# Kernel tuning notes

Hardware: AMD Instinct MI355X
Metric: run time of the kernel (lower is better)

Reference implementation:

```python
import jax, jax.numpy as jnp
import numpy as np

N_NODES = 50000
N_EDGES = 600000
IN_DIM = 128
HID_DIM = 128


def setup_inputs() -> dict:
    key = jax.random.key(0)
    ks = jax.random.split(key, 6)
    x = jax.random.normal(ks[0], (N_NODES, IN_DIM), dtype=jnp.float32)
    edge_index = jax.random.randint(ks[1], (2, N_EDGES), 0, N_NODES, dtype=jnp.int32)
    # GCNConv linear weights (applied as x @ W) and biases
    W1 = jax.random.normal(ks[2], (IN_DIM, HID_DIM), dtype=jnp.float32) * (1.0 / np.sqrt(IN_DIM))
    b1 = jnp.zeros((HID_DIM,), dtype=jnp.float32)
    W2 = jax.random.normal(ks[3], (HID_DIM, HID_DIM), dtype=jnp.float32) * (1.0 / np.sqrt(HID_DIM))
    b2 = jnp.zeros((HID_DIM,), dtype=jnp.float32)
    return {"x": x, "edge_index": edge_index, "W1": W1, "b1": b1, "W2": W2, "b2": b2}


def _gcn_norm(edge_index, num_nodes):
    # add self-loops (edge_weight=None -> all ones), symmetric normalization
    loop = jnp.arange(num_nodes, dtype=edge_index.dtype)
    src = jnp.concatenate([edge_index[0], loop])  # [E+N]
    dst = jnp.concatenate([edge_index[1], loop])  # [E+N]
    ew = jnp.ones(src.shape[0], dtype=jnp.float32)
    deg = jax.ops.segment_sum(ew, dst, num_segments=num_nodes)  # in-degree incl. self-loop
    dinv = jnp.where(deg > 0, jax.lax.rsqrt(deg), 0.0)
    norm = dinv[src] * ew * dinv[dst]  # [E+N]
    return src, dst, norm


def _gcn_layer(z, W, b, src, dst, norm, num_nodes):
    h = z @ W  # [N, H] dense transform
    msg = h[src] * norm[:, None]  # gather + scale  [E+N, H]
    agg = jax.ops.segment_sum(msg, dst, num_segments=num_nodes)  # scatter-add [N, H]
    return agg + b


def reference(x, edge_index, W1, b1, W2, b2):
    num_nodes = x.shape[0]
    src, dst, norm = _gcn_norm(edge_index, num_nodes)
    z = jax.nn.relu(_gcn_layer(x, W1, b1, src, dst, norm, num_nodes))
    z = jax.nn.relu(_gcn_layer(z, W2, b2, src, dst, norm, num_nodes))
    return z
```

## Files before the change

### kernel.cpp

```cpp
#include <hip/hip_runtime.h>

#define NN 50000
#define NE 600000
#define DIM 128
#define CAP 40

#define OFF_CUR    0
#define OFF_DINV   200704
#define OFF_FLAG   401408
#define OFF_SRCL   401920
#define OFF_W1T    8401920
#define OFF_W2T    8434688
#define OFF_Y      8467456
#define OFF_Z1     21267968

typedef unsigned short u16;
typedef unsigned int u32;
typedef __attribute__((ext_vector_type(8))) short short8;
typedef __attribute__((ext_vector_type(4))) float floatx4;

__device__ __forceinline__ float bflo(u32 u) { return __uint_as_float(u << 16); }
__device__ __forceinline__ float bfhi(u32 u) { return __uint_as_float(u & 0xFFFF0000u); }
__device__ __forceinline__ u16 f2bf(float f) {
    u32 x = __float_as_uint(f);
    return (u16)((x + 0x7FFFu + ((x >> 16) & 1u)) >> 16);
}
__device__ __forceinline__ u32 pack2(float hi, float lo) {
    return ((u32)f2bf(hi) << 16) | (u32)f2bf(lo);
}

__global__ __launch_bounds__(256) void k_init(
    const int* __restrict__ ei, const float* __restrict__ W1,
    const float* __restrict__ W2, char* __restrict__ ws) {
    int* cur = (int*)(ws + OFF_CUR);
    int* flagw = (int*)(ws + OFF_FLAG);
    u16* W1t = (u16*)(ws + OFF_W1T);
    u16* W2t = (u16*)(ws + OFF_W2T);
    int b = blockIdx.x, tid = threadIdx.x;
    for (int i = b * 256 + tid; i < NN; i += 128 * 256) cur[i] = 0;
    const float* W = (b < 64) ? W1 : W2;
    u16* Wt = (b < 64) ? W1t : W2t;
    int e = (b & 63) * 256 + tid;
    int k = e >> 7, n = e & 127;
    Wt[n * DIM + k] = f2bf(W[e]);
    if (b == 0) {
        __shared__ int sc;
        if (tid == 0) sc = 0;
        __syncthreads();
        int lc = 0;
        for (int i = tid; i < 1024; i += 256) lc += (ei[2 * i + 1] != 0) ? 1 : 0;
        if (lc) atomicAdd(&sc, lc);
        __syncthreads();
        if (tid == 0) *flagw = (sc < 16) ? 1 : 0;
    }
}

__global__ __launch_bounds__(256) void k_fill(const int* __restrict__ ei,
                                              char* __restrict__ ws) {
    int* cur = (int*)(ws + OFF_CUR);
    int* srclist = (int*)(ws + OFF_SRCL);
    int is64 = *(const int*)(ws + OFF_FLAG);
    int i = blockIdx.x * 256 + threadIdx.x;
    if (i >= NE) return;
    int d = is64 ? ei[2 * (NE + i)] : ei[NE + i];
    if ((u32)d >= NN) return;
    int p = atomicAdd(&cur[d], 1);
    if (p < CAP) {
        int s = is64 ? ei[2 * i] : ei[i];
        srclist[d * CAP + p] = ((u32)s < NN) ? s : 0;
    }
}

__global__ __launch_bounds__(256) void k_scale(const float* __restrict__ x,
                                               char* __restrict__ ws) {
    const int* cur = (const int*)(ws + OFF_CUR);
    float* dinv = (float*)(ws + OFF_DINV);
    u32* y = (u32*)(ws + OFF_Y);
    int i = blockIdx.x * 256 + threadIdx.x;
    if (i >= NN * 32) return;
    int n = i >> 5;
    float dn = rsqrtf((float)(cur[n] + 1));
    if ((i & 31) == 0) dinv[n] = dn;
    float4 v = ((const float4*)x)[i];
    uint2 o;
    o.x = pack2(dn * v.y, dn * v.x);
    o.y = pack2(dn * v.w, dn * v.z);
    ((uint2*)y)[i] = o;
}

__global__ __launch_bounds__(256) void k_layer(
    const u32* __restrict__ y, const char* __restrict__ ws,
    const u16* __restrict__ Bt, const float* __restrict__ bias,
    void* __restrict__ out, int mode) {
    const int* cur = (const int*)(ws + OFF_CUR);
    const int* srclist = (const int*)(ws + OFF_SRCL);
    const float* dinv = (const float*)(ws + OFF_DINV);
    __shared__ u32 tl[16][68];
    int tid = threadIdx.x;
    int wv = tid >> 6, lane = tid & 63;
    int grp = lane >> 4, sl16 = lane & 15;
    int node0 = blockIdx.x << 4;
    int nn = wv * 4 + grp;
    int n = node0 + nn;
    int cnt = cur[n];
    cnt = cnt < CAP ? cnt : CAP;
    float dn = dinv[n];
    const int* sl = srclist + (size_t)n * CAP;
    int c1 = cnt > 0 ? cnt - 1 : 0;

    uint4 us = *(const uint4*)(y + (size_t)n * 64 + sl16 * 4);
    float a0 = bflo(us.x), a1 = bfhi(us.x), a2 = bflo(us.y), a3 = bfhi(us.y);
    float a4 = bflo(us.z), a5 = bfhi(us.z), a6 = bflo(us.w), a7 = bfhi(us.w);

    int mx = cnt;
    mx = max(mx, __shfl_xor(mx, 16));
    mx = max(mx, __shfl_xor(mx, 32));

#define SIDX(j) ((j) < cnt ? sl[(j) < c1 ? (j) : c1] : n)
#define ROW(s) (*(const uint4*)(y + (size_t)(s) * 64 + sl16 * 4))
#define MSK(j) (((j) < cnt) ? 0xFFFFFFFFu : 0u)
    if (mx > 0) {
        int s0 = SIDX(0), s1 = SIDX(1), s2 = SIDX(2), s3 = SIDX(3);
        u32 m0 = MSK(0), m1 = MSK(1), m2 = MSK(2), m3 = MSK(3);
        uint4 u0 = ROW(s0), u1 = ROW(s1), u2 = ROW(s2);
        int sF = s3;
#pragma unroll 2
        for (int i = 0; i < mx; ++i) {
            int sN = SIDX(i + 4);
            uint4 u3 = ROW(sF);
            u32 v;
            v = u0.x & m0; a0 += bflo(v); a1 += bfhi(v);
            v = u0.y & m0; a2 += bflo(v); a3 += bfhi(v);
            v = u0.z & m0; a4 += bflo(v); a5 += bfhi(v);
            v = u0.w & m0; a6 += bflo(v); a7 += bfhi(v);
            u0 = u1; u1 = u2; u2 = u3;
            m0 = m1; m1 = m2; m2 = m3; m3 = MSK(i + 4);
            sF = sN;
        }
    }
#undef SIDX
#undef ROW
#undef MSK
    uint4 o;
    o.x = pack2(dn * a1, dn * a0);
    o.y = pack2(dn * a3, dn * a2);
    o.z = pack2(dn * a5, dn * a4);
    o.w = pack2(dn * a7, dn * a6);
    *(uint4*)&tl[nn][sl16 * 4] = o;
    __syncthreads();

    int m = lane & 15, kg = lane >> 4;
    floatx4 acc[2];
    acc[0] = (floatx4){0.f, 0.f, 0.f, 0.f};
    acc[1] = (floatx4){0.f, 0.f, 0.f, 0.f};
#pragma unroll
    for (int kk = 0; kk < 4; ++kk) {
        int k0 = kk * 32 + kg * 8;
        short8 a = *(const short8*)&tl[m][kk * 16 + kg * 4];
#pragma unroll
        for (int j = 0; j < 2; ++j) {
            int nt = wv * 2 + j;
            short8 b = *(const short8*)(Bt + (size_t)(nt * 16 + m) * DIM + k0);
            acc[j] = __builtin_amdgcn_mfma_f32_16x16x32_bf16(a, b, acc[j], 0, 0, 0);
        }
    }
    float4 d4 = (mode == 0) ? *(const float4*)(dinv + node0 + kg * 4)
                            : make_float4(1.f, 1.f, 1.f, 1.f);
#pragma unroll
    for (int j = 0; j < 2; ++j) {
        int col = (wv * 2 + j) * 16 + m;
        float bv = bias[col];
#pragma unroll
        for (int r = 0; r < 4; ++r) {
            int row = node0 + kg * 4 + r;
            float v = acc[j][r] + bv;
            v = v > 0.f ? v : 0.f;
            if (mode == 0)
                ((u16*)out)[(size_t)row * DIM + col] = f2bf(v * (&d4.x)[r]);
            else
                ((float*)out)[(size_t)row * DIM + col] = v;
        }
    }
}

extern "C" void kernel_launch(void* const* d_in, const int* in_sizes, int n_in,
                              void* d_out, int out_size, void* d_ws, size_t ws_size,
                              hipStream_t stream) {
    (void)in_sizes; (void)n_in; (void)out_size; (void)ws_size;
    const float* x  = (const float*)d_in[0];
    const int*   ei = (const int*)d_in[1];
    const float* W1 = (const float*)d_in[2];
    const float* b1 = (const float*)d_in[3];
    const float* W2 = (const float*)d_in[4];
    const float* b2 = (const float*)d_in[5];
    char* ws = (char*)d_ws;

    u16* W1t = (u16*)(ws + OFF_W1T);
    u16* W2t = (u16*)(ws + OFF_W2T);
    u32* y   = (u32*)(ws + OFF_Y);
    u32* z1  = (u32*)(ws + OFF_Z1);

    k_init<<<128, 256, 0, stream>>>(ei, W1, W2, ws);
    k_fill<<<(NE + 255) / 256, 256, 0, stream>>>(ei, ws);
    k_scale<<<NN * 32 / 256, 256, 0, stream>>>(x, ws);
    k_layer<<<NN / 16, 256, 0, stream>>>(y, ws, W1t, b1, z1, 0);
    k_layer<<<NN / 16, 256, 0, stream>>>(z1, ws, W2t, b2, d_out, 1);
}
```

Measured before the change: 194.2 us.

## Fuse edge fill with bf16 packing and compute source degree scaling in layer one

Merges the CSR fill and x-to-bf16 pack kernels into one launch, which is possible because the pack no longer needs degrees: x is packed unscaled. The first layer instead reads each source node's count and applies rsqrt per gathered neighbor, and all dinv values are recomputed from counts, so the dinv array is gone. This saves a launch and a pass over the data, but adds a dependent gather of cur[src] plus an rsqrt per edge in layer one's inner loop.

```diff
diff --git a/kernel.cpp b/kernel.cpp
--- a/kernel.cpp
+++ b/kernel.cpp
@@ -6,7 +6,6 @@
 #define CAP 40
 
 #define OFF_CUR    0
-#define OFF_DINV   200704
 #define OFF_FLAG   401408
 #define OFF_SRCL   401920
 #define OFF_W1T    8401920
@@ -29,7 +28,7 @@
     return ((u32)f2bf(hi) << 16) | (u32)f2bf(lo);
 }
 
-__global__ __launch_bounds__(256) void k_init(
+__global__ __launch_bounds__(256) void k_z(
     const int* __restrict__ ei, const float* __restrict__ W1,
     const float* __restrict__ W2, char* __restrict__ ws) {
     int* cur = (int*)(ws + OFF_CUR);
@@ -55,37 +54,28 @@
     }
 }
 
-__global__ __launch_bounds__(256) void k_fill(const int* __restrict__ ei,
-                                              char* __restrict__ ws) {
+__global__ __launch_bounds__(256) void k_fillpack(const int* __restrict__ ei,
+                                                  const float* __restrict__ x,
+                                                  char* __restrict__ ws) {
     int* cur = (int*)(ws + OFF_CUR);
     int* srclist = (int*)(ws + OFF_SRCL);
-    int is64 = *(const int*)(ws + OFF_FLAG);
-    int i = blockIdx.x * 256 + threadIdx.x;
-    if (i >= NE) return;
-    int d = is64 ? ei[2 * (NE + i)] : ei[NE + i];
-    if ((u32)d >= NN) return;
-    int p = atomicAdd(&cur[d], 1);
-    if (p < CAP) {
-        int s = is64 ? ei[2 * i] : ei[i];
-        srclist[d * CAP + p] = ((u32)s < NN) ? s : 0;
-    }
-}
-
-__global__ __launch_bounds__(256) void k_scale(const float* __restrict__ x,
-                                               char* __restrict__ ws) {
-    const int* cur = (const int*)(ws + OFF_CUR);
-    float* dinv = (float*)(ws + OFF_DINV);
-    u32* y = (u32*)(ws + OFF_Y);
-    int i = blockIdx.x * 256 + threadIdx.x;
-    if (i >= NN * 32) return;
-    int n = i >> 5;
-    float dn = rsqrtf((float)(cur[n] + 1));
-    if ((i & 31) == 0) dinv[n] = dn;
-    float4 v = ((const float4*)x)[i];
+    int gid = blockIdx.x * 256 + threadIdx.x;
+    float4 v = ((const float4*)x)[gid];
     uint2 o;
-    o.x = pack2(dn * v.y, dn * v.x);
-    o.y = pack2(dn * v.w, dn * v.z);
-    ((uint2*)y)[i] = o;
+    o.x = pack2(v.y, v.x);
+    o.y = pack2(v.w, v.z);
+    ((uint2*)(ws + OFF_Y))[gid] = o;
+    if (gid < NE) {
+        int is64 = *(const int*)(ws + OFF_FLAG);
+        int d = is64 ? ei[2 * (NE + gid)] : ei[NE + gid];
+        if ((u32)d < NN) {
+            int p = atomicAdd(&cur[d], 1);
+            if (p < CAP) {
+                int s = is64 ? ei[2 * gid] : ei[gid];
+                srclist[d * CAP + p] = ((u32)s < NN) ? s : 0;
+            }
+        }
+    }
 }
 
 __global__ __launch_bounds__(256) void k_layer(
@@ -94,7 +84,6 @@
     void* __restrict__ out, int mode) {
     const int* cur = (const int*)(ws + OFF_CUR);
     const int* srclist = (const int*)(ws + OFF_SRCL);
-    const float* dinv = (const float*)(ws + OFF_DINV);
     __shared__ u32 tl[16][68];
     int tid = threadIdx.x;
     int wv = tid >> 6, lane = tid & 63;
@@ -102,15 +91,18 @@
     int node0 = blockIdx.x << 4;
     int nn = wv * 4 + grp;
     int n = node0 + nn;
-    int cnt = cur[n];
-    cnt = cnt < CAP ? cnt : CAP;
-    float dn = dinv[n];
+    int craw = cur[n];
+    float dn = rsqrtf((float)(craw + 1));
+    int cnt = craw < CAP ? craw : CAP;
     const int* sl = srclist + (size_t)n * CAP;
     int c1 = cnt > 0 ? cnt - 1 : 0;
 
     uint4 us = *(const uint4*)(y + (size_t)n * 64 + sl16 * 4);
-    float a0 = bflo(us.x), a1 = bfhi(us.x), a2 = bflo(us.y), a3 = bfhi(us.y);
-    float a4 = bflo(us.z), a5 = bfhi(us.z), a6 = bflo(us.w), a7 = bfhi(us.w);
+    float sw = (mode == 0) ? dn : 1.0f;
+    float a0 = sw * bflo(us.x), a1 = sw * bfhi(us.x);
+    float a2 = sw * bflo(us.y), a3 = sw * bfhi(us.y);
+    float a4 = sw * bflo(us.z), a5 = sw * bfhi(us.z);
+    float a6 = sw * bflo(us.w), a7 = sw * bfhi(us.w);
 
     int mx = cnt;
     mx = max(mx, __shfl_xor(mx, 16));
@@ -123,19 +115,40 @@
         int s0 = SIDX(0), s1 = SIDX(1), s2 = SIDX(2), s3 = SIDX(3);
         u32 m0 = MSK(0), m1 = MSK(1), m2 = MSK(2), m3 = MSK(3);
         uint4 u0 = ROW(s0), u1 = ROW(s1), u2 = ROW(s2);
-        int sF = s3;
+        if (mode == 0) {
+            int c0 = cur[s0], c1v = cur[s1], c2v = cur[s2];
+            int sF = s3;
 #pragma unroll 2
-        for (int i = 0; i < mx; ++i) {
-            int sN = SIDX(i + 4);
-            uint4 u3 = ROW(sF);
-            u32 v;
-            v = u0.x & m0; a0 += bflo(v); a1 += bfhi(v);
-            v = u0.y & m0; a2 += bflo(v); a3 += bfhi(v);
-            v = u0.z & m0; a4 += bflo(v); a5 += bfhi(v);
-            v = u0.w & m0; a6 += bflo(v); a7 += bfhi(v);
-            u0 = u1; u1 = u2; u2 = u3;
-            m0 = m1; m1 = m2; m2 = m3; m3 = MSK(i + 4);
-            sF = sN;
+            for (int i = 0; i < mx; ++i) {
+                int sN = SIDX(i + 4);
+                uint4 u3 = ROW(sF);
+                int c3v = cur[sF];
+                float ds = rsqrtf((float)(c0 + 1));
+                u32 v;
+                v = u0.x & m0; a0 += ds * bflo(v); a1 += ds * bfhi(v);
+                v = u0.y & m0; a2 += ds * bflo(v); a3 += ds * bfhi(v);
+                v = u0.z & m0; a4 += ds * bflo(v); a5 += ds * bfhi(v);
+                v = u0.w & m0; a6 += ds * bflo(v); a7 += ds * bfhi(v);
+                u0 = u1; u1 = u2; u2 = u3;
+                c0 = c1v; c1v = c2v; c2v = c3v;
+                m0 = m1; m1 = m2; m2 = m3; m3 = MSK(i + 4);
+                sF = sN;
+            }
+        } else {
+            int sF = s3;
+#pragma unroll 2
+            for (int i = 0; i < mx; ++i) {
+                int sN = SIDX(i + 4);
+                uint4 u3 = ROW(sF);
+                u32 v;
+                v = u0.x & m0; a0 += bflo(v); a1 += bfhi(v);
+                v = u0.y & m0; a2 += bflo(v); a3 += bfhi(v);
+                v = u0.z & m0; a4 += bflo(v); a5 += bfhi(v);
+                v = u0.w & m0; a6 += bflo(v); a7 += bfhi(v);
+                u0 = u1; u1 = u2; u2 = u3;
+                m0 = m1; m1 = m2; m2 = m3; m3 = MSK(i + 4);
+                sF = sN;
+            }
         }
     }
 #undef SIDX
@@ -164,8 +177,14 @@
             acc[j] = __builtin_amdgcn_mfma_f32_16x16x32_bf16(a, b, acc[j], 0, 0, 0);
         }
     }
-    float4 d4 = (mode == 0) ? *(const float4*)(dinv + node0 + kg * 4)
-                            : make_float4(1.f, 1.f, 1.f, 1.f);
+    float4 d4 = make_float4(1.f, 1.f, 1.f, 1.f);
+    if (mode == 0) {
+        int4 cr = *(const int4*)(cur + node0 + kg * 4);
+        d4.x = rsqrtf((float)(cr.x + 1));
+        d4.y = rsqrtf((float)(cr.y + 1));
+        d4.z = rsqrtf((float)(cr.z + 1));
+        d4.w = rsqrtf((float)(cr.w + 1));
+    }
 #pragma unroll
     for (int j = 0; j < 2; ++j) {
         int col = (wv * 2 + j) * 16 + m;
@@ -200,9 +219,8 @@
     u32* y   = (u32*)(ws + OFF_Y);
     u32* z1  = (u32*)(ws + OFF_Z1);
 
-    k_init<<<128, 256, 0, stream>>>(ei, W1, W2, ws);
-    k_fill<<<(NE + 255) / 256, 256, 0, stream>>>(ei, ws);
-    k_scale<<<NN * 32 / 256, 256, 0, stream>>>(x, ws);
+    k_z<<<128, 256, 0, stream>>>(ei, W1, W2, ws);
+    k_fillpack<<<NN * 32 / 256, 256, 0, stream>>>(ei, x, ws);
     k_layer<<<NN / 16, 256, 0, stream>>>(y, ws, W1t, b1, z1, 0);
     k_layer<<<NN / 16, 256, 0, stream>>>(z1, ws, W2t, b2, d_out, 1);
 }
```

After: 204.2 us. 5.2% more time.
